# Optimization experiments

Hardware: AMD Instinct MI355X
Metric: run time of the kernel (lower is better)

Reference implementation:

```python
import jax, jax.numpy as jnp
import numpy as np

DT = 1.0
S = 64            # num_sites
D = 2 * S         # state_dim
LOG_2PI = float(np.log(2.0 * np.pi))

def _selectors():
    s0 = np.zeros((2, 4), np.float32); s0[:, 0:2] = np.eye(2)
    s1 = np.zeros((2, 4), np.float32); s1[:, 2:4] = np.eye(2)
    cr = 0.5 * (s0 + s1)
    # [target=2, source=2, 2, 4]; off-diagonal pairs use the averaged selector
    return jnp.asarray(np.stack([np.stack([s0, cr]), np.stack([cr, s1])]))

SEL = _selectors()

def project_lon_lat(lon, lat):
    # lon, lat: [B,S]
    lat0 = lat.mean(-1, keepdims=True)
    lon0 = lon.mean(-1, keepdims=True)
    km = 111.32
    x = (lon - lon0) * (km * jnp.cos(jnp.deg2rad(lat0)))
    y = (lat - lat0) * km
    coords = jnp.stack([x, y], -1)                        # [B,S,2]
    h = coords[:, :, None, :] - coords[:, None, :, :]
    dist = jnp.sqrt((h ** 2).sum(-1) + 1e-12)
    npos = (dist > 1e-6).sum((-1, -2)).astype(coords.dtype)
    scale = dist.sum((-1, -2)) / jnp.maximum(npos, 1.0)
    return coords / jnp.maximum(scale, 1e-6)[:, None, None]

def build_A(h, mu, sigma, coupling, damping, eyeD):
    # h: [B,S,S,2], mu: [B,4], sigma: [B,4,4]
    B = mu.shape[0]
    sigma = 0.5 * (sigma + jnp.swapaxes(sigma, -1, -2))
    dm = jnp.einsum('tsab,nb->tsna', SEL, mu)                     # [2,2,B,2]
    dc = jnp.einsum('tsab,nbc,tsdc->tsnad', SEL, sigma, SEL)      # [2,2,B,2,2]
    dc = 0.5 * (dc + jnp.swapaxes(dc, -1, -2))
    eye2 = jnp.eye(2, dtype=h.dtype)
    Dm = (1.0 + 1e-4) * eye2 + (2.0 * DT ** 2) * dc
    Dinv = jnp.linalg.inv(Dm)
    _, logdet = jnp.linalg.slogdet(Dm)
    diff = h[None, None] - DT * dm[:, :, :, None, None, :]        # [2,2,B,S,S,2]
    q = jnp.einsum('tsbijd,tsbdf,tsbijf->tsbij', diff, Dinv, diff)
    ker = jnp.exp(-0.5 * (q + logdet[..., None, None]))
    ker = ker / jnp.maximum(ker.sum(-1, keepdims=True), 1e-6)
    ker = jnp.moveaxis(ker, 2, 0)                                 # [B,2,2,S,S]
    op = ker * coupling[None, :, :, None, None]
    op = jnp.transpose(op, (0, 1, 3, 2, 4)).reshape(B, D, D)
    return eyeD + DT * (op - damping * eyeD)

def _update(m, P, z_t, r2, eyeD):
    # Kalman measurement update with H = I, R = r2*I; returns per-sample NLL term
    Sm = P + r2 * eyeD
    v = z_t - m
    Sinv_v = jnp.linalg.solve(Sm, v[..., None])[..., 0]
    _, logdet = jnp.linalg.slogdet(Sm)
    nll_t = 0.5 * ((v * Sinv_v).sum(-1) + logdet + D * LOG_2PI)
    K = jnp.swapaxes(jnp.linalg.solve(Sm, P), -1, -2)   # P @ Sm^{-1} (P, Sm symmetric)
    m = m + jnp.einsum('bij,bj->bi', K, v)
    P = jnp.einsum('bij,bjk->bik', eyeD - K, P)
    return m, P, nll_t

def reference(z_seq, site_lon, site_lat, mu_seq, sigma_seq,
              log_q_proc, log_r_obs, log_p0, log_damping,
              init_mean, coupling_raw):
    B, T = z_seq.shape[0], z_seq.shape[1]
    z = z_seq.reshape(B, T, D)
    dtype = z.dtype
    eyeD = jnp.eye(D, dtype=dtype)
    r2 = jnp.exp(log_r_obs) ** 2
    q2 = jnp.exp(log_q_proc) ** 2
    damping = jnp.exp(log_damping)
    coupling = jnp.eye(2, dtype=dtype) + 0.25 * jnp.tanh(coupling_raw)

    lon = jnp.broadcast_to(site_lon[None], (B, S))
    lat = jnp.broadcast_to(site_lat[None], (B, S))
    coords = project_lon_lat(lon, lat)
    h = coords[:, :, None, :] - coords[:, None, :, :]   # [B,S,S,2]

    m0 = jnp.broadcast_to(init_mean[None], (B, D))
    P0 = jnp.broadcast_to(jnp.exp(log_p0) ** 2 * eyeD, (B, D, D))
    m, P, nll0 = _update(m0, P0, z[:, 0], r2, eyeD)

    def step(carry, xs):
        m, P = carry
        mu_t, sigma_t, z_t = xs
        A = build_A(h, mu_t, sigma_t, coupling, damping, eyeD)
        m = jnp.einsum('bij,bj->bi', A, m)
        P = jnp.einsum('bij,bjk,blk->bil', A, P, A) + q2 * eyeD
        m, P, nll_t = _update(m, P, z_t, r2, eyeD)
        return (m, P), nll_t

    xs = (jnp.swapaxes(mu_seq, 0, 1), jnp.swapaxes(sigma_seq, 0, 1),
          jnp.swapaxes(z[:, 1:], 0, 1))
    (_, _), nll_rest = jax.lax.scan(step, (m, P), xs)
    nll = nll0 + nll_rest.sum(0)   # [B]
    return nll.mean()

def setup_inputs() -> dict:
    key = jax.random.key(0)
    ks = jax.random.split(key, 5)
    B, T = 16, 128
    z_seq = jax.random.normal(ks[0], (B, T, S, 2), jnp.float32)
    site_lon = 10.0 + 0.5 * jax.random.uniform(ks[1], (S,), jnp.float32)
    site_lat = 55.0 + 0.5 * jax.random.uniform(ks[2], (S,), jnp.float32)
    mu_seq = 0.5 * jax.random.normal(ks[3], (B, T - 1, 4), jnp.float32)
    L = 0.2 * jax.random.normal(ks[4], (B, T - 1, 4, 4), jnp.float32)
    sigma_seq = jnp.einsum('btij,btkj->btik', L, L)   # PSD covariances
    return {
        'z_seq': z_seq, 'site_lon': site_lon, 'site_lat': site_lat,
        'mu_seq': mu_seq, 'sigma_seq': sigma_seq,
        'log_q_proc': jnp.float32(-2.0), 'log_r_obs': jnp.float32(-2.0),
        'log_p0': jnp.float32(0.0), 'log_damping': jnp.float32(0.0),
        'init_mean': jnp.zeros((D,), jnp.float32),
        'coupling_raw': jnp.zeros((2, 2), jnp.float32),
    }
```

## Files before the change

kernel.cpp:

```cpp
#include <hip/hip_runtime.h>
#include <math.h>


#define SQ 64
#define DQ 128
#define TQ 128
#define BQ 16
#define LDP 132
#define LDB 136
#define WFLOATS 17408
#define NTH 1024
#define LOG2PI 1.8378770664093454f

#define SMEM_FLOATS 35472

typedef __attribute__((ext_vector_type(8))) short bf16x8;
typedef __attribute__((ext_vector_type(4))) float f32x4;

__device__ __forceinline__ void lds_fence() {
  __asm__ volatile("s_waitcnt lgkmcnt(0)" ::: "memory");
}

__device__ __forceinline__ unsigned short f2bf(float f) {
  unsigned u = __float_as_uint(f);
  u += 0x7fffu + ((u >> 16) & 1u);
  return (unsigned short)(u >> 16);
}
__device__ __forceinline__ uint4 pack8(const float* v) {
  uint4 r;
  r.x = (unsigned)f2bf(v[0]) | ((unsigned)f2bf(v[1]) << 16);
  r.y = (unsigned)f2bf(v[2]) | ((unsigned)f2bf(v[3]) << 16);
  r.z = (unsigned)f2bf(v[4]) | ((unsigned)f2bf(v[5]) << 16);
  r.w = (unsigned)f2bf(v[6]) | ((unsigned)f2bf(v[7]) << 16);
  return r;
}

__device__ __forceinline__ float block_reduce_sum(float v, float* red) {
  #pragma unroll
  for (int off = 32; off > 0; off >>= 1) v += __shfl_down(v, off);
  const int tid = threadIdx.x;
  if ((tid & 63) == 0) red[tid >> 6] = v;
  __syncthreads();
  v = 0.0f;
  #pragma unroll
  for (int w = 0; w < NTH / 64; w++) v += red[w];
  __syncthreads();
  return v;
}

__device__ __forceinline__ void chol16_f(float* __restrict__ Wf,
                                         float* __restrict__ mdiag,
                                         int b0, int lane) {
  float a[16];
  if (lane < 16) {
    const float4* rp = (const float4*)(Wf + (b0 + lane) * LDP + b0);
    float4 q0 = rp[0], q1 = rp[1], q2v = rp[2], q3 = rp[3];
    a[0]=q0.x; a[1]=q0.y; a[2]=q0.z; a[3]=q0.w;
    a[4]=q1.x; a[5]=q1.y; a[6]=q1.z; a[7]=q1.w;
    a[8]=q2v.x; a[9]=q2v.y; a[10]=q2v.z; a[11]=q2v.w;
    a[12]=q3.x; a[13]=q3.y; a[14]=q3.z; a[15]=q3.w;
  } else {
    #pragma unroll
    for (int i = 0; i < 16; i++) a[i] = 1.0f;
  }
  float myrinv = 1.0f;
  #pragma unroll
  for (int j = 0; j < 16; j++) {
    float dj = __shfl(a[j], j);
    float rinv = rsqrtf(dj);
    float lij = a[j] * rinv;
    a[j] = lij;
    if (lane == j) myrinv = rinv;
    #pragma unroll
    for (int k = j + 1; k < 16; k++) {
      float lkj = __shfl(lij, k);
      a[k] = fmaf(-lij, lkj, a[k]);
    }
  }
  if (lane < 16) {
    float4* rp = (float4*)(Wf + (b0 + lane) * LDP + b0);
    rp[0] = make_float4(a[0], a[1], a[2], a[3]);
    rp[1] = make_float4(a[4], a[5], a[6], a[7]);
    rp[2] = make_float4(a[8], a[9], a[10], a[11]);
    rp[3] = make_float4(a[12], a[13], a[14], a[15]);
    mdiag[b0 + lane] = myrinv;
  }
}

__device__ __forceinline__ void trinv_chain2(float* __restrict__ Wf,
                                             const float* __restrict__ mdiag,
                                             int J, int pass, int lane) {
  const int c16 = lane & 15;
  const int j16 = 4 * (lane >> 4) + pass;
  const int sh = lane & 48;
  {
    float row[16];
    const float4* rp = (const float4*)(Wf + (J * 16 + c16) * LDP + J * 16);
    float4 a0 = rp[0], a1 = rp[1], a2 = rp[2], a3 = rp[3];
    row[0]=a0.x; row[1]=a0.y; row[2]=a0.z; row[3]=a0.w;
    row[4]=a1.x; row[5]=a1.y; row[6]=a1.z; row[7]=a1.w;
    row[8]=a2.x; row[9]=a2.y; row[10]=a2.z; row[11]=a2.w;
    row[12]=a3.x; row[13]=a3.y; row[14]=a3.z; row[15]=a3.w;
    float s = (c16 == j16) ? 1.0f : 0.0f;
    #pragma unroll
    for (int k = 0; k < 16; k++) {
      if (c16 == k) s *= mdiag[J * 16 + k];
      float sk = __shfl(s, sh | k);
      if (c16 > k) s = fmaf(-row[k], sk, s);
    }
    if (c16 > j16) Wf[(J * 16 + j16) * LDP + (J * 16 + c16)] = s;
  }
  lds_fence();
  const float md = mdiag[J * 16 + j16];
  const float* Mrow = Wf + (J * 16 + j16) * LDP + J * 16;
  #pragma unroll 1
  for (int I = J + 1; I < 8; I++) {
    const float* Lrow = Wf + (I * 16 + c16) * LDP + J * 16;
    float g = 0.0f;
    #pragma unroll
    for (int c4 = 0; c4 < 4; c4++) {
      float4 lv = *(const float4*)&Lrow[c4 * 4];
      float4 mq = *(const float4*)&Mrow[c4 * 4];
      float w0 = (c4*4+0 > j16) ? mq.x : ((c4*4+0 == j16) ? md : 0.0f);
      float w1 = (c4*4+1 > j16) ? mq.y : ((c4*4+1 == j16) ? md : 0.0f);
      float w2 = (c4*4+2 > j16) ? mq.z : ((c4*4+2 == j16) ? md : 0.0f);
      float w3 = (c4*4+3 > j16) ? mq.w : ((c4*4+3 == j16) ? md : 0.0f);
      g = fmaf(lv.x, w0, g); g = fmaf(lv.y, w1, g);
      g = fmaf(lv.z, w2, g); g = fmaf(lv.w, w3, g);
    }
    for (int K = J + 1; K < I; K++) {
      const float* LK = Lrow + (K - J) * 16;
      const float* MK = Wf + (J * 16 + j16) * LDP + K * 16;
      #pragma unroll
      for (int c4 = 0; c4 < 4; c4++) {
        float4 lv = *(const float4*)&LK[c4 * 4];
        float4 mq = *(const float4*)&MK[c4 * 4];
        g = fmaf(lv.x, mq.x, g); g = fmaf(lv.y, mq.y, g);
        g = fmaf(lv.z, mq.z, g); g = fmaf(lv.w, mq.w, g);
      }
    }
    float row2[16];
    {
      const float4* rp2 = (const float4*)(Wf + (I * 16 + c16) * LDP + I * 16);
      float4 a0 = rp2[0], a1 = rp2[1], a2 = rp2[2], a3 = rp2[3];
      row2[0]=a0.x; row2[1]=a0.y; row2[2]=a0.z; row2[3]=a0.w;
      row2[4]=a1.x; row2[5]=a1.y; row2[6]=a1.z; row2[7]=a1.w;
      row2[8]=a2.x; row2[9]=a2.y; row2[10]=a2.z; row2[11]=a2.w;
      row2[12]=a3.x; row2[13]=a3.y; row2[14]=a3.z; row2[15]=a3.w;
    }
    float sv = g;
    #pragma unroll
    for (int k = 0; k < 16; k++) {
      if (c16 == k) sv *= mdiag[I * 16 + k];
      float sk = __shfl(sv, sh | k);
      if (c16 > k) sv = fmaf(-row2[k], sk, sv);
    }
    Wf[(J * 16 + j16) * LDP + (I * 16 + c16)] = -sv;
    lds_fence();
  }
}

extern "C" __global__ __launch_bounds__(NTH, 4)
void ide_kf_kernel(const float* __restrict__ z_seq,
                   const float* __restrict__ site_lon,
                   const float* __restrict__ site_lat,
                   const float* __restrict__ mu_seq,
                   const float* __restrict__ sigma_seq,
                   const float* __restrict__ log_q,
                   const float* __restrict__ log_r,
                   const float* __restrict__ log_p0,
                   const float* __restrict__ log_damp,
                   const float* __restrict__ init_mean,
                   const float* __restrict__ coupling_raw,
                   float* __restrict__ ws) {
  extern __shared__ float smem[];
  float* Wf     = smem;
  float* B1f    = Wf + WFLOATS;
  float* B2f    = B1f + 8704;
  float* coords = B2f + 8704;
  float* mv     = coords + 128;
  float* vv     = mv + DQ;
  float* yv     = vv + DQ;
  float* mdiag  = yv + DQ;
  float* red    = mdiag + DQ;

  unsigned short* Tb  = (unsigned short*)Wf;
  unsigned short* Ab2 = (unsigned short*)Wf + 17408;
  unsigned short* Mtb = (unsigned short*)B1f;
  unsigned short* Pb  = (unsigned short*)B2f;
  unsigned short* Lhi = (unsigned short*)B1f;
  unsigned short* Llo = (unsigned short*)B2f;

  const int tid = threadIdx.x;
  const int lane = tid & 63;
  const int wave = tid >> 6;
  const int rb = wave >> 1, ch = wave & 1;
  const int m16 = lane & 15, quad = lane >> 4;
  const int grp = wave >> 2, pass = wave & 3;
  const int b = blockIdx.x;
  float* nll_out = ws;

  const float r2 = __expf(2.0f * log_r[0]);
  const float q2 = __expf(2.0f * log_q[0]);
  const float p0sq = __expf(2.0f * log_p0[0]);
  const float damping = __expf(log_damp[0]);
  const float cpl00 = 1.0f + 0.25f * tanhf(coupling_raw[0]);
  const float cpl01 = 0.25f * tanhf(coupling_raw[1]);
  const float cpl10 = 0.25f * tanhf(coupling_raw[2]);
  const float cpl11 = 1.0f + 0.25f * tanhf(coupling_raw[3]);

  float myLon = (tid < SQ) ? site_lon[tid] : 0.0f;
  float myLat = (tid < SQ) ? site_lat[tid] : 0.0f;
  float lat0 = block_reduce_sum(myLat, red) * (1.0f / 64.0f);
  float lon0 = block_reduce_sum(myLon, red) * (1.0f / 64.0f);
  if (tid < SQ) {
    const float km = 111.32f;
    float cs = cosf(lat0 * 0.017453292519943295f);
    coords[2 * tid]     = (myLon - lon0) * (km * cs);
    coords[2 * tid + 1] = (myLat - lat0) * km;
  }
  __syncthreads();
  float dsum = 0.0f, dcnt = 0.0f;
  for (int idx = tid; idx < SQ * SQ; idx += NTH) {
    int i = idx >> 6, j = idx & 63;
    float dx = coords[2 * i] - coords[2 * j];
    float dy = coords[2 * i + 1] - coords[2 * j + 1];
    float d = sqrtf(dx * dx + dy * dy + 1e-12f);
    dsum += d;
    if (d > 1e-6f) dcnt += 1.0f;
  }
  dsum = block_reduce_sum(dsum, red);
  dcnt = block_reduce_sum(dcnt, red);
  float scale = dsum / fmaxf(dcnt, 1.0f);
  float sdiv = 1.0f / fmaxf(scale, 1e-6f);
  if (tid < SQ) { coords[2 * tid] *= sdiv; coords[2 * tid + 1] *= sdiv; }

  for (int e = tid; e < WFLOATS / 4; e += NTH)
    ((float4*)Wf)[e] = make_float4(0.0f, 0.0f, 0.0f, 0.0f);
  for (int e = tid; e < 8704 / 4; e += NTH)
    ((float4*)B2f)[e] = make_float4(0.0f, 0.0f, 0.0f, 0.0f);
  __syncthreads();
  if (tid < DQ) {
    Wf[tid * LDP + tid] = p0sq + r2;
    mv[tid] = init_mean[tid];
  }
  __syncthreads();

  float nllp = 0.0f;

  #pragma unroll 1
  for (int t = 0; t < TQ; t++) {
    const float* zt = z_seq + ((size_t)b * TQ + t) * DQ;

    if (t > 0) {
      {
        f32x4 acc[4];
        #pragma unroll
        for (int c = 0; c < 4; c++) acc[c] = (f32x4){0.0f, 0.0f, 0.0f, 0.0f};
        #pragma unroll
        for (int ks = 0; ks < 4; ks++) {
          const int ko = 32 * ks + 8 * quad;
          bf16x8 a = *(const bf16x8*)(Ab2 + (16 * rb + m16) * LDB + ko);
          #pragma unroll
          for (int ct = 0; ct < 4; ct++) {
            bf16x8 bb = *(const bf16x8*)(Pb + (64 * ch + 16 * ct + m16) * LDB + ko);
            acc[ct] = __builtin_amdgcn_mfma_f32_16x16x32_bf16(a, bb, acc[ct], 0, 0, 0);
          }
        }
        #pragma unroll
        for (int ct = 0; ct < 4; ct++)
          #pragma unroll
          for (int reg = 0; reg < 4; reg++)
            Tb[(16 * rb + 4 * quad + reg) * LDB + 64 * ch + 16 * ct + m16] =
                f2bf(acc[ct][reg]);
        __syncthreads();
      }

      {
        const int ctmax = rb - 4 * ch;
        f32x4 acc[4];
        #pragma unroll
        for (int c = 0; c < 4; c++) acc[c] = (f32x4){0.0f, 0.0f, 0.0f, 0.0f};
        const bool gemv_wave = (wave == 1 || wave == 3);
        const int grow = (wave == 1) ? lane : 64 + lane;
        float newm = 0.0f;
        if (ctmax >= 0) {
          #pragma unroll
          for (int ks = 0; ks < 4; ks++) {
            const int ko = 32 * ks + 8 * quad;
            bf16x8 a = *(const bf16x8*)(Tb + (16 * rb + m16) * LDB + ko);
            #pragma unroll
            for (int ct = 0; ct < 4; ct++) {
              if (ct <= ctmax) {
                bf16x8 bb = *(const bf16x8*)(Ab2 + (64 * ch + 16 * ct + m16) * LDB + ko);
                acc[ct] = __builtin_amdgcn_mfma_f32_16x16x32_bf16(a, bb, acc[ct], 0, 0, 0);
              }
            }
          }
        } else if (gemv_wave) {
          const unsigned* ar = (const unsigned*)(Ab2 + grow * LDB);
          #pragma unroll 8
          for (int k2 = 0; k2 < 64; k2++) {
            unsigned p = ar[k2];
            newm = fmaf(__uint_as_float(p << 16), mv[2 * k2], newm);
            newm = fmaf(__uint_as_float(p & 0xffff0000u), mv[2 * k2 + 1], newm);
          }
        }
        __syncthreads();
        if (ctmax >= 0) {
          #pragma unroll
          for (int ct = 0; ct < 4; ct++) {
            if (ct <= ctmax) {
              #pragma unroll
              for (int reg = 0; reg < 4; reg++) {
                const int rg = 16 * rb + 4 * quad + reg;
                const int cgl = 64 * ch + 16 * ct + m16;
                Wf[rg * LDP + cgl] = acc[ct][reg] + ((rg == cgl) ? (q2 + r2) : 0.0f);
              }
            }
          }
        }
        if (gemv_wave) vv[grow] = zt[grow] - newm;
        if (wave == 0) {
          lds_fence();
          chol16_f(Wf, mdiag, 0, lane);
        }
        __syncthreads();
      }
    }

    if (t == 0) {
      if (tid < 64) {
        chol16_f(Wf, mdiag, 0, lane);
      } else if (tid < 192) {
        const int i = tid - 64;
        vv[i] = zt[i] - mv[i];
      }
      __syncthreads();
    }

    #pragma unroll 1
    for (int kb = 0; kb < 7; kb++) {
      const int b0k = kb * 16, base = b0k + 16, nbelow = DQ - base;
      if (tid < nbelow) {
        const int r = base + tid;
        float* wr = Wf + r * LDP + b0k;
        float w[16];
        #pragma unroll
        for (int u4 = 0; u4 < 4; u4++) {
          float4 w4 = *(const float4*)&wr[u4 * 4];
          w[u4*4] = w4.x; w[u4*4+1] = w4.y; w[u4*4+2] = w4.z; w[u4*4+3] = w4.w;
        }
        #pragma unroll
        for (int j = 0; j < 16; j++) {
          float s = w[j];
          #pragma unroll
          for (int l = 0; l < 16; l++) {
            if (l < j) s = fmaf(-w[l], Wf[(b0k + j) * LDP + b0k + l], s);
          }
          w[j] = s * mdiag[b0k + j];
        }
        #pragma unroll
        for (int u4 = 0; u4 < 4; u4++)
          *(float4*)&wr[u4 * 4] =
              make_float4(w[u4*4], w[u4*4+1], w[u4*4+2], w[u4*4+3]);
        unsigned short hs[16]; float lo[16];
        #pragma unroll
        for (int u = 0; u < 16; u++) {
          hs[u] = f2bf(w[u]);
          lo[u] = w[u] - __uint_as_float(((unsigned)hs[u]) << 16);
        }
        uint4 h0, h1;
        h0.x = hs[0] | ((unsigned)hs[1] << 16);   h0.y = hs[2] | ((unsigned)hs[3] << 16);
        h0.z = hs[4] | ((unsigned)hs[5] << 16);   h0.w = hs[6] | ((unsigned)hs[7] << 16);
        h1.x = hs[8] | ((unsigned)hs[9] << 16);   h1.y = hs[10] | ((unsigned)hs[11] << 16);
        h1.z = hs[12] | ((unsigned)hs[13] << 16); h1.w = hs[14] | ((unsigned)hs[15] << 16);
        unsigned short* hr = Lhi + r * LDB + b0k;
        unsigned short* lr = Llo + r * LDB + b0k;
        *(uint4*)(hr) = h0; *(uint4*)(hr + 8) = h1;
        *(uint4*)(lr) = pack8(lo); *(uint4*)(lr + 8) = pack8(lo + 8);
        const uint4 z4 = make_uint4(0u, 0u, 0u, 0u);
        *(uint4*)(hr + 16) = z4; *(uint4*)(hr + 24) = z4;
        *(uint4*)(lr + 16) = z4; *(uint4*)(lr + 24) = z4;
      }
      __syncthreads();
      if (wave <= 6 - kb) {
        const int bi = kb + 1 + wave;
        const int nch = (kb + 2) >> 1;
        f32x4 acc = (f32x4){0.0f, 0.0f, 0.0f, 0.0f};
        for (int c = 0; c < nch; c++) {
          const int ko = 32 * c + 8 * quad;
          bf16x8 ahi = *(const bf16x8*)(Lhi + (16 * bi + m16) * LDB + ko);
          bf16x8 alo = *(const bf16x8*)(Llo + (16 * bi + m16) * LDB + ko);
          bf16x8 bhi = *(const bf16x8*)(Lhi + (base + m16) * LDB + ko);
          bf16x8 blo = *(const bf16x8*)(Llo + (base + m16) * LDB + ko);
          acc = __builtin_amdgcn_mfma_f32_16x16x32_bf16(ahi, bhi, acc, 0, 0, 0);
          acc = __builtin_amdgcn_mfma_f32_16x16x32_bf16(ahi, blo, acc, 0, 0, 0);
          acc = __builtin_amdgcn_mfma_f32_16x16x32_bf16(alo, bhi, acc, 0, 0, 0);
        }
        #pragma unroll
        for (int reg = 0; reg < 4; reg++)
          Wf[(16 * bi + 4 * quad + reg) * LDP + base + m16] -= acc[reg];
        if (wave == 0) {
          lds_fence();
          chol16_f(Wf, mdiag, base, lane);
        }
      }
      __syncthreads();
    }

    {
      #pragma unroll 1
      for (int cc = 0; cc < 2; cc++) {
        const int J = cc ? (7 - grp) : grp;
        trinv_chain2(Wf, mdiag, J, pass, lane);
      }
      __syncthreads();
    }

    {
      const int mrow = tid >> 3, kc = (tid & 7) * 16;
      float mtv[16];
      if (kc > mrow) {
        const float4* rp = (const float4*)(Wf + mrow * LDP + kc);
        float4 q0 = rp[0], q1 = rp[1], q2v = rp[2], q3 = rp[3];
        mtv[0]=q0.x; mtv[1]=q0.y; mtv[2]=q0.z; mtv[3]=q0.w;
        mtv[4]=q1.x; mtv[5]=q1.y; mtv[6]=q1.z; mtv[7]=q1.w;
        mtv[8]=q2v.x; mtv[9]=q2v.y; mtv[10]=q2v.z; mtv[11]=q2v.w;
        mtv[12]=q3.x; mtv[13]=q3.y; mtv[14]=q3.z; mtv[15]=q3.w;
      } else if (kc + 15 < mrow) {
        #pragma unroll
        for (int u = 0; u < 16; u++) mtv[u] = 0.0f;
      } else {
        #pragma unroll
        for (int u = 0; u < 16; u++) {
          const int k = kc + u;
          mtv[u] = (k > mrow) ? Wf[mrow * LDP + k]
                 : ((k == mrow) ? mdiag[mrow] : 0.0f);
        }
      }
      if (tid < DQ) {
        nllp -= __logf(mdiag[tid]);
        float s = mdiag[tid] * vv[tid];
        for (int k = 0; k < tid; k++) s = fmaf(Wf[k * LDP + tid], vv[k], s);
        yv[tid] = s;
      }
      unsigned short* mt = Mtb + mrow * LDB + kc;
      *(uint4*)(mt) = pack8(mtv);
      *(uint4*)(mt + 8) = pack8(mtv + 8);
      __syncthreads();
    }

    {
      f32x4 acc[4];
      #pragma unroll
      for (int c = 0; c < 4; c++) acc[c] = (f32x4){0.0f, 0.0f, 0.0f, 0.0f};
      if (tid < DQ) nllp += 0.5f * yv[tid] * yv[tid];
      const int ctmax = rb - 4 * ch;
      if (ctmax >= 0) {
        for (int ks = (rb >> 1); ks < 4; ks++) {
          const int ko = 32 * ks + 8 * quad;
          bf16x8 a = *(const bf16x8*)(Mtb + (16 * rb + m16) * LDB + ko);
          #pragma unroll
          for (int ct = 0; ct < 4; ct++) {
            if (ct <= ctmax) {
              bf16x8 bb = *(const bf16x8*)(Mtb + (64 * ch + 16 * ct + m16) * LDB + ko);
              acc[ct] = __builtin_amdgcn_mfma_f32_16x16x32_bf16(a, bb, acc[ct], 0, 0, 0);
            }
          }
        }
      }
      const float nr22 = -r2 * r2;
      #pragma unroll
      for (int ct = 0; ct < 4; ct++) {
        if (ct <= ctmax) {
          const bool strict = (ct < ctmax);
          #pragma unroll
          for (int reg = 0; reg < 4; reg++) {
            const int rg = 16 * rb + 4 * quad + reg;
            const int cgl = 64 * ch + 16 * ct + m16;
            unsigned short hv = f2bf(nr22 * acc[ct][reg] + ((rg == cgl) ? r2 : 0.0f));
            Pb[rg * LDB + cgl] = hv;
            if (strict) Pb[cgl * LDB + rg] = hv;
          }
        }
      }
      if (tid < DQ) {
        const unsigned* mr = (const unsigned*)(Mtb + tid * LDB);
        float s = 0.0f;
        #pragma unroll 8
        for (int k2 = 0; k2 < 64; k2++) {
          unsigned p = mr[k2];
          s = fmaf(__uint_as_float(p << 16), yv[2 * k2], s);
          s = fmaf(__uint_as_float(p & 0xffff0000u), yv[2 * k2 + 1], s);
        }
        mv[tid] = zt[tid] - r2 * s;
      }
      if (t < TQ - 1) {
        const float* mu_t = mu_seq + ((size_t)b * (TQ - 1) + t) * 4;
        const float* sg_t = sigma_seq + ((size_t)b * (TQ - 1) + t) * 16;
        const int unit = tid >> 2, q = tid & 3;
        const int r = unit >> 1, ss = unit & 1, tt = r >> 6, i = r & 63;
        float m0 = mu_t[0], m1 = mu_t[1], m2 = mu_t[2], m3 = mu_t[3];
        float dmx, dmy, c00, c01, c11;
        if (tt == 0 && ss == 0) {
          dmx = m0; dmy = m1;
          c00 = sg_t[0]; c01 = 0.5f * (sg_t[1] + sg_t[4]); c11 = sg_t[5];
        } else if (tt == 1 && ss == 1) {
          dmx = m2; dmy = m3;
          c00 = sg_t[10]; c01 = 0.5f * (sg_t[11] + sg_t[14]); c11 = sg_t[15];
        } else {
          dmx = 0.5f * (m0 + m2); dmy = 0.5f * (m1 + m3);
          float s00 = sg_t[0];
          float s02 = 0.5f * (sg_t[2] + sg_t[8]);
          float s22 = sg_t[10];
          float s01 = 0.5f * (sg_t[1] + sg_t[4]);
          float s03 = 0.5f * (sg_t[3] + sg_t[12]);
          float s21 = 0.5f * (sg_t[9] + sg_t[6]);
          float s23 = 0.5f * (sg_t[11] + sg_t[14]);
          float s11 = sg_t[5];
          float s13 = 0.5f * (sg_t[7] + sg_t[13]);
          float s33 = sg_t[15];
          c00 = 0.25f * (s00 + s02 + s02 + s22);
          c01 = 0.25f * (s01 + s03 + s21 + s23);
          c11 = 0.25f * (s11 + s13 + s13 + s33);
        }
        float D00 = 1.0001f + 2.0f * c00;
        float D01 = 2.0f * c01;
        float D11 = 1.0001f + 2.0f * c11;
        float det = D00 * D11 - D01 * D01;
        float dinv = 1.0f / det;
        float d00 = D11 * dinv, d01 = -D01 * dinv, d11 = D00 * dinv;
        float ldts = __logf(det);
        float cix = coords[2 * i], ciy = coords[2 * i + 1];
        const float* cj = coords + q * 32;
        float kv[16];
        float rsum = 0.0f;
        #pragma unroll
        for (int u = 0; u < 16; u++) {
          float dx = cix - cj[2 * u] - dmx;
          float dy = ciy - cj[2 * u + 1] - dmy;
          float qf = d00 * dx * dx + 2.0f * d01 * dx * dy + d11 * dy * dy;
          kv[u] = __expf(-0.5f * (qf + ldts));
          rsum += kv[u];
        }
        float rtot = rsum + __shfl_xor(rsum, 1);
        rtot += __shfl_xor(rtot, 2);
        float cv = (tt == 0) ? ((ss == 0) ? cpl00 : cpl01)
                             : ((ss == 0) ? cpl10 : cpl11);
        float norm = cv / fmaxf(rtot, 1e-6f);
        #pragma unroll
        for (int u = 0; u < 16; u++) kv[u] *= norm;
        if (ss == tt && ((i >> 4) == q)) kv[i & 15] += 1.0f - damping;
        unsigned short* arow = Ab2 + r * LDB + ss * 64 + q * 16;
        *(uint4*)(arow) = pack8(kv);
        *(uint4*)(arow + 8) = pack8(kv + 8);
      }
      __syncthreads();
    }
  }

  float total = block_reduce_sum(nllp, red);
  if (tid == 0)
    nll_out[b] = total + (float)TQ * 0.5f * (float)DQ * LOG2PI;
}

extern "C" __global__ void ide_finalize(const float* __restrict__ part,
                                        float* __restrict__ out) {
  if (threadIdx.x == 0) {
    float s = 0.0f;
    for (int i = 0; i < BQ; i++) s += part[i];
    out[0] = s * (1.0f / BQ);
  }
}

extern "C" void kernel_launch(void* const* d_in, const int* in_sizes, int n_in,
                              void* d_out, int out_size, void* d_ws, size_t ws_size,
                              hipStream_t stream) {
  (void)in_sizes; (void)n_in; (void)out_size; (void)ws_size;
  const float* z_seq        = (const float*)d_in[0];
  const float* site_lon     = (const float*)d_in[1];
  const float* site_lat     = (const float*)d_in[2];
  const float* mu_seq       = (const float*)d_in[3];
  const float* sigma_seq    = (const float*)d_in[4];
  const float* log_q        = (const float*)d_in[5];
  const float* log_r        = (const float*)d_in[6];
  const float* log_p0       = (const float*)d_in[7];
  const float* log_damp     = (const float*)d_in[8];
  const float* init_mean    = (const float*)d_in[9];
  const float* coupling_raw = (const float*)d_in[10];
  float* ws = (float*)d_ws;
  float* out = (float*)d_out;

  const size_t smem_bytes = (size_t)SMEM_FLOATS * sizeof(float);
  hipFuncSetAttribute((const void*)ide_kf_kernel,
                      hipFuncAttributeMaxDynamicSharedMemorySize,
                      (int)smem_bytes);

  hipLaunchKernelGGL(ide_kf_kernel, dim3(BQ), dim3(NTH), smem_bytes, stream,
                     z_seq, site_lon, site_lat, mu_seq, sigma_seq,
                     log_q, log_r, log_p0, log_damp, init_mean, coupling_raw,
                     ws);
  hipLaunchKernelGGL(ide_finalize, dim3(1), dim3(64), 0, stream, ws, out);
}
```

Measured before the change: 8.354 ms.

## Overlap diagonal-block triangular inverse with Cholesky panel and split dot-product accumulators

During the blocked Cholesky loop, idle waves 4-7 now invert the just-factored 16x16 diagonal block while other waves pack the panel to bf16. The later triangular-inverse phase skips that step for blocks already handled and only runs it for the last block. The serial forward-substitution dot product and the Mtb*y reduction now use multiple independent accumulators to shorten FMA dependency chains. Summation order changes slightly, and correctness relies on which blocks the overlapped inversion covers, so the block indexing has to line up exactly.

```diff
diff --git a/kernel.cpp b/kernel.cpp
--- a/kernel.cpp
+++ b/kernel.cpp
@@ -89,11 +89,12 @@
 
 __device__ __forceinline__ void trinv_chain2(float* __restrict__ Wf,
                                              const float* __restrict__ mdiag,
-                                             int J, int pass, int lane) {
+                                             int J, int pass, int lane,
+                                             bool do1) {
   const int c16 = lane & 15;
   const int j16 = 4 * (lane >> 4) + pass;
   const int sh = lane & 48;
-  {
+  if (do1) {
     float row[16];
     const float4* rp = (const float4*)(Wf + (J * 16 + c16) * LDP + J * 16);
     float4 a0 = rp[0], a1 = rp[1], a2 = rp[2], a3 = rp[3];
@@ -109,8 +110,8 @@
       if (c16 > k) s = fmaf(-row[k], sk, s);
     }
     if (c16 > j16) Wf[(J * 16 + j16) * LDP + (J * 16 + c16)] = s;
-  }
-  lds_fence();
+    lds_fence();
+  }
   const float md = mdiag[J * 16 + j16];
   const float* Mrow = Wf + (J * 16 + j16) * LDP + J * 16;
   #pragma unroll 1
@@ -382,6 +383,25 @@
         const uint4 z4 = make_uint4(0u, 0u, 0u, 0u);
         *(uint4*)(hr + 16) = z4; *(uint4*)(hr + 24) = z4;
         *(uint4*)(lr + 16) = z4; *(uint4*)(lr + 24) = z4;
+      } else if (wave >= 4 && wave <= 7) {
+        const int c16 = lane & 15;
+        const int j16 = 4 * (lane >> 4) + (wave - 4);
+        const int sh = lane & 48;
+        float row[16];
+        const float4* rp = (const float4*)(Wf + (b0k + c16) * LDP + b0k);
+        float4 a0 = rp[0], a1 = rp[1], a2 = rp[2], a3 = rp[3];
+        row[0]=a0.x; row[1]=a0.y; row[2]=a0.z; row[3]=a0.w;
+        row[4]=a1.x; row[5]=a1.y; row[6]=a1.z; row[7]=a1.w;
+        row[8]=a2.x; row[9]=a2.y; row[10]=a2.z; row[11]=a2.w;
+        row[12]=a3.x; row[13]=a3.y; row[14]=a3.z; row[15]=a3.w;
+        float s = (c16 == j16) ? 1.0f : 0.0f;
+        #pragma unroll
+        for (int k = 0; k < 16; k++) {
+          if (c16 == k) s *= mdiag[b0k + k];
+          float sk = __shfl(s, sh | k);
+          if (c16 > k) s = fmaf(-row[k], sk, s);
+        }
+        if (c16 > j16) Wf[(b0k + j16) * LDP + (b0k + c16)] = s;
       }
       __syncthreads();
       if (wave <= 6 - kb) {
@@ -410,11 +430,8 @@
     }
 
     {
-      #pragma unroll 1
-      for (int cc = 0; cc < 2; cc++) {
-        const int J = cc ? (7 - grp) : grp;
-        trinv_chain2(Wf, mdiag, J, pass, lane);
-      }
+      trinv_chain2(Wf, mdiag, grp, pass, lane, false);
+      trinv_chain2(Wf, mdiag, 7 - grp, pass, lane, grp == 0);
       __syncthreads();
     }
 
@@ -441,8 +458,16 @@
       }
       if (tid < DQ) {
         nllp -= __logf(mdiag[tid]);
-        float s = mdiag[tid] * vv[tid];
-        for (int k = 0; k < tid; k++) s = fmaf(Wf[k * LDP + tid], vv[k], s);
+        float s0 = 0.0f, s1 = 0.0f, s2 = 0.0f, s3 = 0.0f;
+        int k = 0;
+        for (; k + 3 < tid; k += 4) {
+          s0 = fmaf(Wf[k * LDP + tid], vv[k], s0);
+          s1 = fmaf(Wf[(k + 1) * LDP + tid], vv[k + 1], s1);
+          s2 = fmaf(Wf[(k + 2) * LDP + tid], vv[k + 2], s2);
+          s3 = fmaf(Wf[(k + 3) * LDP + tid], vv[k + 3], s3);
+        }
+        float s = fmaf(mdiag[tid], vv[tid], (s0 + s1) + (s2 + s3));
+        for (; k < tid; k++) s = fmaf(Wf[k * LDP + tid], vv[k], s);
         yv[tid] = s;
       }
       unsigned short* mt = Mtb + mrow * LDB + kc;
@@ -487,14 +512,16 @@
       }
       if (tid < DQ) {
         const unsigned* mr = (const unsigned*)(Mtb + tid * LDB);
-        float s = 0.0f;
+        float sa = 0.0f, sb = 0.0f;
         #pragma unroll 8
-        for (int k2 = 0; k2 < 64; k2++) {
-          unsigned p = mr[k2];
-          s = fmaf(__uint_as_float(p << 16), yv[2 * k2], s);
-          s = fmaf(__uint_as_float(p & 0xffff0000u), yv[2 * k2 + 1], s);
-        }
-        mv[tid] = zt[tid] - r2 * s;
+        for (int k2 = 0; k2 < 64; k2 += 2) {
+          unsigned p0 = mr[k2], p1 = mr[k2 + 1];
+          sa = fmaf(__uint_as_float(p0 << 16), yv[2 * k2], sa);
+          sa = fmaf(__uint_as_float(p0 & 0xffff0000u), yv[2 * k2 + 1], sa);
+          sb = fmaf(__uint_as_float(p1 << 16), yv[2 * k2 + 2], sb);
+          sb = fmaf(__uint_as_float(p1 & 0xffff0000u), yv[2 * k2 + 3], sb);
+        }
+        mv[tid] = zt[tid] - r2 * (sa + sb);
       }
       if (t < TQ - 1) {
         const float* mu_t = mu_seq + ((size_t)b * (TQ - 1) + t) * 4;
```

Result: slower. 8.890 ms (+6.4%).

## Overlap diagonal-block inversion with Cholesky and reuse inverted blocks in trinv chain

Applied to the files above, without the earlier changes.

Idle waves 8-11 now invert each finished 16x16 diagonal Cholesky block during the factorization loop, so trinv_chain2 mostly skips its own diagonal inversion. Off-diagonal block solves for I<7 become a multiply by the precomputed inverse instead of a serial shuffle-based triangular solve. This shortens the serial dependency chain in the triangular inverse. In exchange it adds work and register pressure in the Cholesky phase, and correctness depends on the ordering of block writes.

```diff
diff --git a/kernel.cpp b/kernel.cpp
--- a/kernel.cpp
+++ b/kernel.cpp
@@ -89,11 +89,12 @@
 
 __device__ __forceinline__ void trinv_chain2(float* __restrict__ Wf,
                                              const float* __restrict__ mdiag,
-                                             int J, int pass, int lane) {
+                                             int J, int pass, int lane,
+                                             bool do1) {
   const int c16 = lane & 15;
   const int j16 = 4 * (lane >> 4) + pass;
   const int sh = lane & 48;
-  {
+  if (do1) {
     float row[16];
     const float4* rp = (const float4*)(Wf + (J * 16 + c16) * LDP + J * 16);
     float4 a0 = rp[0], a1 = rp[1], a2 = rp[2], a3 = rp[3];
@@ -109,8 +110,8 @@
       if (c16 > k) s = fmaf(-row[k], sk, s);
     }
     if (c16 > j16) Wf[(J * 16 + j16) * LDP + (J * 16 + c16)] = s;
-  }
-  lds_fence();
+    lds_fence();
+  }
   const float md = mdiag[J * 16 + j16];
   const float* Mrow = Wf + (J * 16 + j16) * LDP + J * 16;
   #pragma unroll 1
@@ -139,23 +140,36 @@
         g = fmaf(lv.z, mq.z, g); g = fmaf(lv.w, mq.w, g);
       }
     }
-    float row2[16];
-    {
-      const float4* rp2 = (const float4*)(Wf + (I * 16 + c16) * LDP + I * 16);
-      float4 a0 = rp2[0], a1 = rp2[1], a2 = rp2[2], a3 = rp2[3];
-      row2[0]=a0.x; row2[1]=a0.y; row2[2]=a0.z; row2[3]=a0.w;
-      row2[4]=a1.x; row2[5]=a1.y; row2[6]=a1.z; row2[7]=a1.w;
-      row2[8]=a2.x; row2[9]=a2.y; row2[10]=a2.z; row2[11]=a2.w;
-      row2[12]=a3.x; row2[13]=a3.y; row2[14]=a3.z; row2[15]=a3.w;
-    }
-    float sv = g;
-    #pragma unroll
-    for (int k = 0; k < 16; k++) {
-      if (c16 == k) sv *= mdiag[I * 16 + k];
-      float sk = __shfl(sv, sh | k);
-      if (c16 > k) sv = fmaf(-row2[k], sk, sv);
-    }
-    Wf[(J * 16 + j16) * LDP + (I * 16 + c16)] = -sv;
+    if (I < 7) {
+      float s = mdiag[I * 16 + c16] * g;
+      #pragma unroll
+      for (int k = 0; k < 15; k++) {
+        float gk = __shfl(g, sh | k);
+        if (k < c16) {
+          float u = Wf[(I * 16 + k) * LDP + I * 16 + c16];
+          s = fmaf(u, gk, s);
+        }
+      }
+      Wf[(J * 16 + j16) * LDP + (I * 16 + c16)] = -s;
+    } else {
+      float row2[16];
+      {
+        const float4* rp2 = (const float4*)(Wf + (I * 16 + c16) * LDP + I * 16);
+        float4 a0 = rp2[0], a1 = rp2[1], a2 = rp2[2], a3 = rp2[3];
+        row2[0]=a0.x; row2[1]=a0.y; row2[2]=a0.z; row2[3]=a0.w;
+        row2[4]=a1.x; row2[5]=a1.y; row2[6]=a1.z; row2[7]=a1.w;
+        row2[8]=a2.x; row2[9]=a2.y; row2[10]=a2.z; row2[11]=a2.w;
+        row2[12]=a3.x; row2[13]=a3.y; row2[14]=a3.z; row2[15]=a3.w;
+      }
+      float sv = g;
+      #pragma unroll
+      for (int k = 0; k < 16; k++) {
+        if (c16 == k) sv *= mdiag[I * 16 + k];
+        float sk = __shfl(sv, sh | k);
+        if (c16 > k) sv = fmaf(-row2[k], sk, sv);
+      }
+      Wf[(J * 16 + j16) * LDP + (I * 16 + c16)] = -sv;
+    }
     lds_fence();
   }
 }
@@ -405,6 +419,25 @@
           lds_fence();
           chol16_f(Wf, mdiag, base, lane);
         }
+      } else if (wave >= 8 && wave <= 11) {
+        const int c16 = lane & 15;
+        const int j16s = 4 * (lane >> 4) + (wave - 8);
+        const int sh = lane & 48;
+        float row[16];
+        const float4* rp = (const float4*)(Wf + (b0k + c16) * LDP + b0k);
+        float4 a0 = rp[0], a1 = rp[1], a2 = rp[2], a3 = rp[3];
+        row[0]=a0.x; row[1]=a0.y; row[2]=a0.z; row[3]=a0.w;
+        row[4]=a1.x; row[5]=a1.y; row[6]=a1.z; row[7]=a1.w;
+        row[8]=a2.x; row[9]=a2.y; row[10]=a2.z; row[11]=a2.w;
+        row[12]=a3.x; row[13]=a3.y; row[14]=a3.z; row[15]=a3.w;
+        float s = (c16 == j16s) ? 1.0f : 0.0f;
+        #pragma unroll
+        for (int k = 0; k < 16; k++) {
+          if (c16 == k) s *= mdiag[b0k + k];
+          float sk = __shfl(s, sh | k);
+          if (c16 > k) s = fmaf(-row[k], sk, s);
+        }
+        if (c16 > j16s) Wf[(b0k + j16s) * LDP + (b0k + c16)] = s;
       }
       __syncthreads();
     }
@@ -413,7 +446,7 @@
       #pragma unroll 1
       for (int cc = 0; cc < 2; cc++) {
         const int J = cc ? (7 - grp) : grp;
-        trinv_chain2(Wf, mdiag, J, pass, lane);
+        trinv_chain2(Wf, mdiag, J, pass, lane, cc == 1 && grp == 0);
       }
       __syncthreads();
     }
```

After: 7.806 ms, median of 2. -6.6%, faster.
